# Optimization experiments

Measured on AMD Instinct MI355X. Metric: run time of the kernel, lower is better.

The kernel has to match this reference:

```python
import jax, jax.numpy as jnp
import numpy as np

SEARCH_RANGE = 4  # matches argv.search_range


def setup_inputs() -> dict:
    key = jax.random.key(0)
    k1, k2 = jax.random.split(key)
    B, C, H, W = 8, 128, 128, 128
    first = jax.random.normal(k1, (B, C, H, W), dtype=jnp.float32)
    second = jax.random.normal(k2, (B, C, H, W), dtype=jnp.float32)
    return {"first": first, "second": second}


def reference(first, second):
    r = SEARCH_RANGE
    B, C, H, W = first.shape
    # pad last two dims (H, W) by search_range on each side, zeros
    padded = jnp.pad(second, ((0, 0), (0, 0), (r, r), (r, r)))
    max_offset = 2 * r + 1
    # For each static (y, x) offset, slice the shifted window and reduce over
    # channels: cost[b, y*max_offset + x, h, w] = mean_c first * padded_shifted.
    costs = [
        jnp.mean(first * jax.lax.dynamic_slice(padded, (0, 0, y, x), (B, C, H, W)), axis=1)
        for y in range(max_offset)
        for x in range(max_offset)
    ]
    return jnp.stack(costs, axis=1)  # [B, (2r+1)^2, H, W]
```

## Files before the change

### kernel.cpp

```cpp
#include <hip/hip_runtime.h>


constexpr int B = 8, C = 128, H = 128, W = 128;
constexpr int RNG = 4, MO = 9;
constexpr int RW  = 4;
constexpr int TH  = 2;
constexpr int HWc = H * W;
constexpr int SROWS = TH + 2 * RNG;
constexpr int SLAB  = (TH + SROWS) * W;
constexpr int NBUF  = 4;

typedef float f32x4 __attribute__((ext_vector_type(4)));

__global__ __launch_bounds__(576)
__attribute__((amdgpu_waves_per_eu(2, 5)))
void corr_kernel(const float* __restrict__ first,
                 const float* __restrict__ second,
                 float* __restrict__ out)
{
    const int tx = threadIdx.x;
    const int hy = threadIdx.y;
    const int dz = threadIdx.z;
    const int h0 = blockIdx.x * TH;
    const int b  = blockIdx.y;
    const int w0 = tx * RW;
    const int lane = tx + 32 * hy;

    __shared__ __align__(16) float slab[NBUF][SLAB];

    const float* gsrc = nullptr;
    int ldsoff = 0;
    if (dz == 0) {
        gsrc  = first + (size_t)b * C * HWc + h0 * W + lane * 4;
        ldsoff = 0;
    } else if (dz <= 5) {
        const int p  = dz - 1;
        const int r0 = h0 - RNG + 2 * p;
        const int cs = r0 < 0 ? 0 : (r0 > H - 2 ? H - 2 : r0);
        gsrc  = second + (size_t)b * C * HWc + cs * W + lane * 4;
        ldsoff = (TH + 2 * p) * W;
    }
    const bool do_stage = (dz <= 5);

    const int  srow   = h0 + hy + dz - RNG;
    const bool rvalid = (srow >= 0) && (srow < H);
    const bool ledge  = (tx == 0);
    const bool redge  = (tx == 31);
    const int off0  = ledge ? 0       : (w0 - 4);
    const int off2  = redge ? (W - 8) : (w0 + 4);
    const int fbase = hy * W + w0;
    const int sbase = (TH + hy + dz) * W;

    float acc[MO][RW];
#pragma unroll
    for (int i = 0; i < MO; ++i)
#pragma unroll
        for (int p = 0; p < RW; ++p) acc[i][p] = 0.0f;

#define STAGE(k)                                                            \
    if (do_stage) {                                                         \
        __builtin_amdgcn_global_load_lds(                                   \
            (const __attribute__((address_space(1))) void*)                 \
                (gsrc + (size_t)(k) * HWc),                                 \
            (__attribute__((address_space(3))) void*)                       \
                (&slab[(k) & (NBUF - 1)][ldsoff]),                          \
            16, 0, 0);                                                      \
    }

    STAGE(0)
    STAGE(1)

    for (int k = 0; k < C; ++k) {
        if (k < C - 2) {
            STAGE(k + 2)
            asm volatile("s_waitcnt vmcnt(2)" ::: "memory");
        } else if (k == C - 2) {
            asm volatile("s_waitcnt vmcnt(1)" ::: "memory");
        } else {
            asm volatile("s_waitcnt vmcnt(0)" ::: "memory");
        }
        __builtin_amdgcn_s_barrier();

        const float* sb = slab[k & (NBUF - 1)];
        f32x4 fv = *(const f32x4*)(sb + fbase);
        f32x4 a0 = *(const f32x4*)(sb + sbase + off0);
        f32x4 a1 = *(const f32x4*)(sb + sbase + w0);
        f32x4 a2 = *(const f32x4*)(sb + sbase + off2);
        if (ledge) a0 = (f32x4){0.f, 0.f, 0.f, 0.f};
        if (redge) a2 = (f32x4){0.f, 0.f, 0.f, 0.f};
        const float s[12] = {a0.x, a0.y, a0.z, a0.w,
                             a1.x, a1.y, a1.z, a1.w,
                             a2.x, a2.y, a2.z, a2.w};
        const float fvv[RW] = {fv.x, fv.y, fv.z, fv.w};
#pragma unroll
        for (int dx = 0; dx < MO; ++dx)
#pragma unroll
            for (int p = 0; p < RW; ++p)
                acc[dx][p] += fvv[p] * s[p + dx];

        asm volatile("s_waitcnt lgkmcnt(0)" ::: "memory");
        __builtin_amdgcn_sched_barrier(0);
    }
#undef STAGE

    const float inv = rvalid ? (1.0f / (float)C) : 0.0f;
    float* obase = out + ((size_t)b * (MO * MO) + (size_t)dz * MO) * HWc
                       + (size_t)(h0 + hy) * W + w0;
#pragma unroll
    for (int dx = 0; dx < MO; ++dx) {
        f32x4 v = {acc[dx][0] * inv, acc[dx][1] * inv,
                   acc[dx][2] * inv, acc[dx][3] * inv};
        *(f32x4*)(obase + (size_t)dx * HWc) = v;
    }
}

extern "C" void kernel_launch(void* const* d_in, const int* in_sizes, int n_in,
                              void* d_out, int out_size, void* d_ws, size_t ws_size,
                              hipStream_t stream) {
    const float* first  = (const float*)d_in[0];
    const float* second = (const float*)d_in[1];
    float* out = (float*)d_out;

    dim3 grid(H / TH, B);
    dim3 block(32, TH, MO);
    corr_kernel<<<grid, block, 0, stream>>>(first, second, out);
}
```

Before: 185.1 us.

## Batch channel staging into 4-channel phases with triple-buffered LDS pipeline

```diff
diff --git a/kernel.cpp b/kernel.cpp
--- a/kernel.cpp
+++ b/kernel.cpp
@@ -6,9 +6,11 @@
 constexpr int RW  = 4;
 constexpr int TH  = 2;
 constexpr int HWc = H * W;
-constexpr int SROWS = TH + 2 * RNG;
-constexpr int SLAB  = (TH + SROWS) * W;
-constexpr int NBUF  = 4;
+constexpr int CPP = 4;
+constexpr int NP  = C / CPP;
+constexpr int PBUF = 3;
+constexpr int SLABR = TH + TH + 2 * RNG;
+constexpr int SLAB  = SLABR * W;
 
 typedef float f32x4 __attribute__((ext_vector_type(4)));
 
@@ -26,7 +28,7 @@
     const int w0 = tx * RW;
     const int lane = tx + 32 * hy;
 
-    __shared__ __align__(16) float slab[NBUF][SLAB];
+    __shared__ __align__(16) float slab[PBUF][CPP][SLAB];
 
     const float* gsrc = nullptr;
     int ldsoff = 0;
@@ -34,11 +36,11 @@
         gsrc  = first + (size_t)b * C * HWc + h0 * W + lane * 4;
         ldsoff = 0;
     } else if (dz <= 5) {
-        const int p  = dz - 1;
-        const int r0 = h0 - RNG + 2 * p;
+        const int q  = dz - 1;
+        const int r0 = h0 - RNG + 2 * q;
         const int cs = r0 < 0 ? 0 : (r0 > H - 2 ? H - 2 : r0);
         gsrc  = second + (size_t)b * C * HWc + cs * W + lane * 4;
-        ldsoff = (TH + 2 * p) * W;
+        ldsoff = (TH + 2 * q) * W;
     }
     const bool do_stage = (dz <= 5);
 
@@ -57,51 +59,70 @@
 #pragma unroll
         for (int p = 0; p < RW; ++p) acc[i][p] = 0.0f;
 
-#define STAGE(k)                                                            \
+#define FENCE asm volatile("" ::: "memory");
+
+#define STAGE1(c, buf)                                                      \
     if (do_stage) {                                                         \
         __builtin_amdgcn_global_load_lds(                                   \
             (const __attribute__((address_space(1))) void*)                 \
-                (gsrc + (size_t)(k) * HWc),                                 \
+                (gsrc + (size_t)(c) * HWc),                                 \
             (__attribute__((address_space(3))) void*)                       \
-                (&slab[(k) & (NBUF - 1)][ldsoff]),                          \
+                (&slab[buf][(c) & (CPP - 1)][ldsoff]),                      \
             16, 0, 0);                                                      \
     }
 
-    STAGE(0)
-    STAGE(1)
+#define STAGEP(p)                                                           \
+    {                                                                       \
+        const int _bp = (p) % PBUF;                                         \
+        STAGE1((p) * CPP + 0, _bp)                                          \
+        STAGE1((p) * CPP + 1, _bp)                                          \
+        STAGE1((p) * CPP + 2, _bp)                                          \
+        STAGE1((p) * CPP + 3, _bp)                                          \
+    }
 
-    for (int k = 0; k < C; ++k) {
-        if (k < C - 2) {
-            STAGE(k + 2)
-            asm volatile("s_waitcnt vmcnt(2)" ::: "memory");
-        } else if (k == C - 2) {
-            asm volatile("s_waitcnt vmcnt(1)" ::: "memory");
-        } else {
-            asm volatile("s_waitcnt vmcnt(0)" ::: "memory");
-        }
+#define COMPUTE_PHASE(p)                                                    \
+    {                                                                       \
+        const float* pb = &slab[(p) % PBUF][0][0];                          \
+        _Pragma("unroll")                                                   \
+        for (int kc = 0; kc < CPP; ++kc) {                                  \
+            const float* sc = pb + kc * SLAB;                               \
+            f32x4 fv = *(const f32x4*)(sc + fbase);                         \
+            f32x4 a0 = *(const f32x4*)(sc + sbase + off0);                  \
+            f32x4 a1 = *(const f32x4*)(sc + sbase + w0);                    \
+            f32x4 a2 = *(const f32x4*)(sc + sbase + off2);                  \
+            if (ledge) a0 = (f32x4){0.f, 0.f, 0.f, 0.f};                    \
+            if (redge) a2 = (f32x4){0.f, 0.f, 0.f, 0.f};                    \
+            const float s[12] = {a0.x, a0.y, a0.z, a0.w,                    \
+                                 a1.x, a1.y, a1.z, a1.w,                    \
+                                 a2.x, a2.y, a2.z, a2.w};                   \
+            const float fvv[RW] = {fv.x, fv.y, fv.z, fv.w};                 \
+            _Pragma("unroll")                                               \
+            for (int dx = 0; dx < MO; ++dx)                                 \
+                _Pragma("unroll")                                           \
+                for (int pp = 0; pp < RW; ++pp)                             \
+                    acc[dx][pp] += fvv[pp] * s[pp + dx];                    \
+        }                                                                   \
+        asm volatile("s_waitcnt lgkmcnt(0)" ::: "memory");                  \
+        __builtin_amdgcn_sched_barrier(0);                                  \
+    }
+
+    STAGEP(0)
+    FENCE
+    STAGEP(1)
+
+    for (int p = 0; p < NP; ++p) {
+        if (p < NP - 1) { asm volatile("s_waitcnt vmcnt(4)" ::: "memory"); }
+        else            { asm volatile("s_waitcnt vmcnt(0)" ::: "memory"); }
+        __builtin_amdgcn_sched_barrier(0);
         __builtin_amdgcn_s_barrier();
+        if (p < NP - 2) STAGEP(p + 2)
+        COMPUTE_PHASE(p)
+    }
 
-        const float* sb = slab[k & (NBUF - 1)];
-        f32x4 fv = *(const f32x4*)(sb + fbase);
-        f32x4 a0 = *(const f32x4*)(sb + sbase + off0);
-        f32x4 a1 = *(const f32x4*)(sb + sbase + w0);
-        f32x4 a2 = *(const f32x4*)(sb + sbase + off2);
-        if (ledge) a0 = (f32x4){0.f, 0.f, 0.f, 0.f};
-        if (redge) a2 = (f32x4){0.f, 0.f, 0.f, 0.f};
-        const float s[12] = {a0.x, a0.y, a0.z, a0.w,
-                             a1.x, a1.y, a1.z, a1.w,
-                             a2.x, a2.y, a2.z, a2.w};
-        const float fvv[RW] = {fv.x, fv.y, fv.z, fv.w};
-#pragma unroll
-        for (int dx = 0; dx < MO; ++dx)
-#pragma unroll
-            for (int p = 0; p < RW; ++p)
-                acc[dx][p] += fvv[p] * s[p + dx];
-
-        asm volatile("s_waitcnt lgkmcnt(0)" ::: "memory");
-        __builtin_amdgcn_sched_barrier(0);
-    }
-#undef STAGE
+#undef COMPUTE_PHASE
+#undef STAGEP
+#undef STAGE1
+#undef FENCE
 
     const float inv = rvalid ? (1.0f / (float)C) : 0.0f;
     float* obase = out + ((size_t)b * (MO * MO) + (size_t)dz * MO) * HWc
```

Result: no change. 186.4 us (+0.7%).

## Load first tensor directly into registers instead of staging through LDS

Applied to the files above, without the earlier changes.

```diff
diff --git a/kernel.cpp b/kernel.cpp
--- a/kernel.cpp
+++ b/kernel.cpp
@@ -7,7 +7,7 @@
 constexpr int TH  = 2;
 constexpr int HWc = H * W;
 constexpr int SROWS = TH + 2 * RNG;
-constexpr int SLAB  = (TH + SROWS) * W;
+constexpr int SLAB  = SROWS * W;
 constexpr int NBUF  = 4;
 
 typedef float f32x4 __attribute__((ext_vector_type(4)));
@@ -28,19 +28,15 @@
 
     __shared__ __align__(16) float slab[NBUF][SLAB];
 
+    const bool do_stage = (dz < 5);
     const float* gsrc = nullptr;
     int ldsoff = 0;
-    if (dz == 0) {
-        gsrc  = first + (size_t)b * C * HWc + h0 * W + lane * 4;
-        ldsoff = 0;
-    } else if (dz <= 5) {
-        const int p  = dz - 1;
-        const int r0 = h0 - RNG + 2 * p;
+    if (do_stage) {
+        const int r0 = h0 - RNG + 2 * dz;
         const int cs = r0 < 0 ? 0 : (r0 > H - 2 ? H - 2 : r0);
         gsrc  = second + (size_t)b * C * HWc + cs * W + lane * 4;
-        ldsoff = (TH + 2 * p) * W;
+        ldsoff = 2 * dz * W;
     }
-    const bool do_stage = (dz <= 5);
 
     const int  srow   = h0 + hy + dz - RNG;
     const bool rvalid = (srow >= 0) && (srow < H);
@@ -48,8 +44,7 @@
     const bool redge  = (tx == 31);
     const int off0  = ledge ? 0       : (w0 - 4);
     const int off2  = redge ? (W - 8) : (w0 + 4);
-    const int fbase = hy * W + w0;
-    const int sbase = (TH + hy + dz) * W;
+    const int sbase = (hy + dz) * W;
 
     float acc[MO][RW];
 #pragma unroll
@@ -67,22 +62,23 @@
             16, 0, 0);                                                      \
     }
 
+    const float* fp = first + (size_t)b * C * HWc + (h0 + hy) * W + w0;
+
+    f32x4 fcur = *(const f32x4*)(fp);
+    fp += HWc;
+
     STAGE(0)
     STAGE(1)
 
     for (int k = 0; k < C; ++k) {
-        if (k < C - 2) {
-            STAGE(k + 2)
-            asm volatile("s_waitcnt vmcnt(2)" ::: "memory");
-        } else if (k == C - 2) {
-            asm volatile("s_waitcnt vmcnt(1)" ::: "memory");
-        } else {
-            asm volatile("s_waitcnt vmcnt(0)" ::: "memory");
-        }
-        __builtin_amdgcn_s_barrier();
+        __syncthreads();
+
+        if (k < C - 2) STAGE(k + 2)
+
+        f32x4 fnxt;
+        if (k < C - 1) { fnxt = *(const f32x4*)(fp); fp += HWc; }
 
         const float* sb = slab[k & (NBUF - 1)];
-        f32x4 fv = *(const f32x4*)(sb + fbase);
         f32x4 a0 = *(const f32x4*)(sb + sbase + off0);
         f32x4 a1 = *(const f32x4*)(sb + sbase + w0);
         f32x4 a2 = *(const f32x4*)(sb + sbase + off2);
@@ -91,15 +87,14 @@
         const float s[12] = {a0.x, a0.y, a0.z, a0.w,
                              a1.x, a1.y, a1.z, a1.w,
                              a2.x, a2.y, a2.z, a2.w};
-        const float fvv[RW] = {fv.x, fv.y, fv.z, fv.w};
+        const float fvv[RW] = {fcur.x, fcur.y, fcur.z, fcur.w};
 #pragma unroll
         for (int dx = 0; dx < MO; ++dx)
 #pragma unroll
             for (int p = 0; p < RW; ++p)
                 acc[dx][p] += fvv[p] * s[p + dx];
 
-        asm volatile("s_waitcnt lgkmcnt(0)" ::: "memory");
-        __builtin_amdgcn_sched_barrier(0);
+        fcur = fnxt;
     }
 #undef STAGE
 
```

Result: slower. 223.4 us (+20.6%).

## Software-pipeline LDS reads one channel ahead and use zero-padded edge slots

Applied to the files above, without the earlier changes.

```diff
diff --git a/kernel.cpp b/kernel.cpp
--- a/kernel.cpp
+++ b/kernel.cpp
@@ -7,13 +7,16 @@
 constexpr int TH  = 2;
 constexpr int HWc = H * W;
 constexpr int SROWS = TH + 2 * RNG;
-constexpr int SLAB  = (TH + SROWS) * W;
+constexpr int SLABR = TH + SROWS;
+constexpr int SLAB  = SLABR * W;
+constexpr int ZOFF  = SLAB;
+constexpr int SLABP = SLAB + 4;
 constexpr int NBUF  = 4;
 
 typedef float f32x4 __attribute__((ext_vector_type(4)));
 
 __global__ __launch_bounds__(576)
-__attribute__((amdgpu_waves_per_eu(2, 5)))
+__attribute__((amdgpu_waves_per_eu(5, 8)))
 void corr_kernel(const float* __restrict__ first,
                  const float* __restrict__ second,
                  float* __restrict__ out)
@@ -26,7 +29,10 @@
     const int w0 = tx * RW;
     const int lane = tx + 32 * hy;
 
-    __shared__ __align__(16) float slab[NBUF][SLAB];
+    __shared__ __align__(16) float slab[NBUF][SLABP];
+
+    if (dz == 0 && hy == 0 && tx < NBUF * 4)
+        slab[tx >> 2][ZOFF + (tx & 3)] = 0.0f;
 
     const float* gsrc = nullptr;
     int ldsoff = 0;
@@ -34,22 +40,21 @@
         gsrc  = first + (size_t)b * C * HWc + h0 * W + lane * 4;
         ldsoff = 0;
     } else if (dz <= 5) {
-        const int p  = dz - 1;
-        const int r0 = h0 - RNG + 2 * p;
+        const int q  = dz - 1;
+        const int r0 = h0 - RNG + 2 * q;
         const int cs = r0 < 0 ? 0 : (r0 > H - 2 ? H - 2 : r0);
         gsrc  = second + (size_t)b * C * HWc + cs * W + lane * 4;
-        ldsoff = (TH + 2 * p) * W;
+        ldsoff = (TH + 2 * q) * W;
     }
     const bool do_stage = (dz <= 5);
 
     const int  srow   = h0 + hy + dz - RNG;
     const bool rvalid = (srow >= 0) && (srow < H);
-    const bool ledge  = (tx == 0);
-    const bool redge  = (tx == 31);
-    const int off0  = ledge ? 0       : (w0 - 4);
-    const int off2  = redge ? (W - 8) : (w0 + 4);
+    const int sbase = (TH + hy + dz) * W;
     const int fbase = hy * W + w0;
-    const int sbase = (TH + hy + dz) * W;
+    const int aoff1 = sbase + w0;
+    const int aoff0 = (tx == 0)  ? ZOFF : (aoff1 - 4);
+    const int aoff2 = (tx == 31) ? ZOFF : (aoff1 + 4);
 
     float acc[MO][RW];
 #pragma unroll
@@ -67,40 +72,69 @@
             16, 0, 0);                                                      \
     }
 
+#define LDSREAD(SET, k)                                                     \
+    {                                                                       \
+        const float* sb = slab[(k) & (NBUF - 1)];                           \
+        f##SET  = *(const f32x4*)(sb + fbase);                              \
+        a0##SET = *(const f32x4*)(sb + aoff0);                              \
+        a1##SET = *(const f32x4*)(sb + aoff1);                              \
+        a2##SET = *(const f32x4*)(sb + aoff2);                              \
+    }
+
+#define COMPUTE(SET)                                                        \
+    {                                                                       \
+        const float s[12]  = {a0##SET.x, a0##SET.y, a0##SET.z, a0##SET.w,   \
+                              a1##SET.x, a1##SET.y, a1##SET.z, a1##SET.w,   \
+                              a2##SET.x, a2##SET.y, a2##SET.z, a2##SET.w};  \
+        const float fvv[RW] = {f##SET.x, f##SET.y, f##SET.z, f##SET.w};     \
+        _Pragma("unroll")                                                   \
+        for (int dx = 0; dx < MO; ++dx)                                     \
+            _Pragma("unroll")                                               \
+            for (int p = 0; p < RW; ++p)                                    \
+                acc[dx][p] += fvv[p] * s[p + dx];                           \
+    }
+
+#define SYNC1                                                               \
+    asm volatile("s_waitcnt vmcnt(1) lgkmcnt(0)" ::: "memory");             \
+    __builtin_amdgcn_sched_barrier(0);                                      \
+    __builtin_amdgcn_s_barrier();
+
+#define SYNC0                                                               \
+    asm volatile("s_waitcnt vmcnt(0) lgkmcnt(0)" ::: "memory");             \
+    __builtin_amdgcn_sched_barrier(0);                                      \
+    __builtin_amdgcn_s_barrier();
+
+#define BODY(k, CUR, NXT)                                                   \
+    {                                                                       \
+        STAGE((k) + 2)                                                      \
+        SYNC1                                        \
+        LDSREAD(NXT, (k) + 1)              \
+        COMPUTE(CUR)                                         \
+    }
+
+    f32x4 fA, a0A, a1A, a2A, fB, a0B, a1B, a2B;
+
     STAGE(0)
     STAGE(1)
+    SYNC1
+    LDSREAD(A, 0)
 
-    for (int k = 0; k < C; ++k) {
-        if (k < C - 2) {
-            STAGE(k + 2)
-            asm volatile("s_waitcnt vmcnt(2)" ::: "memory");
-        } else if (k == C - 2) {
-            asm volatile("s_waitcnt vmcnt(1)" ::: "memory");
-        } else {
-            asm volatile("s_waitcnt vmcnt(0)" ::: "memory");
-        }
-        __builtin_amdgcn_s_barrier();
+    for (int k = 0; k < C - 4; k += 2) {
+        BODY(k,     A, B)
+        BODY(k + 1, B, A)
+    }
+    BODY(C - 4, A, B)
+    BODY(C - 3, B, A)
+    SYNC0
+    LDSREAD(B, C - 1)
+    COMPUTE(A)
+    COMPUTE(B)
 
-        const float* sb = slab[k & (NBUF - 1)];
-        f32x4 fv = *(const f32x4*)(sb + fbase);
-        f32x4 a0 = *(const f32x4*)(sb + sbase + off0);
-        f32x4 a1 = *(const f32x4*)(sb + sbase + w0);
-        f32x4 a2 = *(const f32x4*)(sb + sbase + off2);
-        if (ledge) a0 = (f32x4){0.f, 0.f, 0.f, 0.f};
-        if (redge) a2 = (f32x4){0.f, 0.f, 0.f, 0.f};
-        const float s[12] = {a0.x, a0.y, a0.z, a0.w,
-                             a1.x, a1.y, a1.z, a1.w,
-                             a2.x, a2.y, a2.z, a2.w};
-        const float fvv[RW] = {fv.x, fv.y, fv.z, fv.w};
-#pragma unroll
-        for (int dx = 0; dx < MO; ++dx)
-#pragma unroll
-            for (int p = 0; p < RW; ++p)
-                acc[dx][p] += fvv[p] * s[p + dx];
-
-        asm volatile("s_waitcnt lgkmcnt(0)" ::: "memory");
-        __builtin_amdgcn_sched_barrier(0);
-    }
+#undef BODY
+#undef SYNC0
+#undef SYNC1
+#undef COMPUTE
+#undef LDSREAD
 #undef STAGE
 
     const float inv = rvalid ? (1.0f / (float)C) : 0.0f;
```

New measurement: 239.7 us. 1.29x slower.
